# Performance work log

Hardware: AMD Instinct MI355X
Metric: run time of the kernel (lower is better)

Reference implementation:

```python
import jax, jax.numpy as jnp
import numpy as np

INPUT_SIZE = 784
HIDDEN_SIZE = 256
NUM_CLASSES = 10
BATCH = 32768


def setup_inputs() -> dict:
    key = jax.random.key(0)
    k_x, k_w1, k_b1, k_w2, k_b2 = jax.random.split(key, 5)
    return {
        "x": jax.random.normal(k_x, (BATCH, INPUT_SIZE), dtype=jnp.float32),
        "fc1_weight": jax.random.normal(k_w1, (HIDDEN_SIZE, INPUT_SIZE), dtype=jnp.float32),
        "fc1_bias": jax.random.normal(k_b1, (HIDDEN_SIZE,), dtype=jnp.float32),
        "fc2_weight": jax.random.normal(k_w2, (NUM_CLASSES, HIDDEN_SIZE), dtype=jnp.float32),
        "fc2_bias": jax.random.normal(k_b2, (NUM_CLASSES,), dtype=jnp.float32),
    }


def reference(x, fc1_weight, fc1_bias, fc2_weight, fc2_bias):
    # hidden = x @ W1^T + b1, ReLU
    hidden = jnp.einsum("bi,hi->bh", x, fc1_weight) + fc1_bias
    activated = jnp.maximum(hidden, 0.0)
    # output = activated @ W2^T + b2
    logits = jnp.einsum("bh,ch->bc", activated, fc2_weight) + fc2_bias
    return jax.nn.softmax(logits, axis=-1)
```

## Files before the change

kernel.cpp:

```cpp
#include <hip/hip_runtime.h>
#include <math.h>

#define BATCH_N   32768
#define IN_F      784
#define HID_F     256
#define NCLS      10
#define BM        64
#define NTHREADS  512

typedef __attribute__((ext_vector_type(8))) short short8;
typedef __attribute__((ext_vector_type(4))) float f32x4;

#define WS_W1H 0
#define WS_W1L 409600

union S8U { short8 s; uint4 u; };

__device__ __forceinline__ void cvt8(float4 a, float4 b, short8* hi, short8* lo) {
    const unsigned M = 0xFFFF0000u;
    const unsigned ux = __float_as_uint(a.x), uy = __float_as_uint(a.y),
                   uz = __float_as_uint(a.z), uw = __float_as_uint(a.w),
                   vx = __float_as_uint(b.x), vy = __float_as_uint(b.y),
                   vz = __float_as_uint(b.z), vw = __float_as_uint(b.w);
    S8U h, l;
    h.u.x = (ux >> 16) | (uy & M);
    h.u.y = (uz >> 16) | (uw & M);
    h.u.z = (vx >> 16) | (vy & M);
    h.u.w = (vz >> 16) | (vw & M);
    const float rx = a.x - __uint_as_float(ux & M);
    const float ry = a.y - __uint_as_float(uy & M);
    const float rz = a.z - __uint_as_float(uz & M);
    const float rw = a.w - __uint_as_float(uw & M);
    const float sx = b.x - __uint_as_float(vx & M);
    const float sy = b.y - __uint_as_float(vy & M);
    const float sz = b.z - __uint_as_float(vz & M);
    const float sw_ = b.w - __uint_as_float(vw & M);
    l.u.x = (__float_as_uint(rx) >> 16) | (__float_as_uint(ry) & M);
    l.u.y = (__float_as_uint(rz) >> 16) | (__float_as_uint(rw) & M);
    l.u.z = (__float_as_uint(sx) >> 16) | (__float_as_uint(sy) & M);
    l.u.w = (__float_as_uint(sz) >> 16) | (__float_as_uint(sw_) & M);
    *hi = h.s; *lo = l.s;
}

__global__ __launch_bounds__(256)
void prep_w1_kernel(const float* __restrict__ w1, char* __restrict__ ws) {
    const int s    = blockIdx.x * 256 + threadIdx.x;
    const int lane = s & 63, ct = (s >> 6) & 15, kt = s >> 10;
    const int n    = ct * 16 + (lane & 15);
    const int k0   = kt * 32 + (lane >> 4) * 8;
    float4 a = make_float4(0.f, 0.f, 0.f, 0.f), b = a;
    if (k0 + 7 < IN_F) {
        const float* p = w1 + (size_t)n * IN_F + k0;
        a = *(const float4*)p;
        b = *(const float4*)(p + 4);
    }
    short8 hi, lo;
    cvt8(a, b, &hi, &lo);
    *(short8*)(ws + WS_W1H + (size_t)s * 16) = hi;
    *(short8*)(ws + WS_W1L + (size_t)s * 16) = lo;
}

__device__ __forceinline__ void gload16(const void* g, void* l) {
    __builtin_amdgcn_global_load_lds(
        (const __attribute__((address_space(1))) void*)g,
        (__attribute__((address_space(3))) void*)l, 16, 0, 0);
}

__device__ __forceinline__ short8 gload_s8(const void* p) {
    short8 r;
    asm volatile("global_load_dwordx4 %0, %1, off" : "=v"(r) : "v"(p));
    return r;
}

__global__ __launch_bounds__(NTHREADS, 2)
void mlp_mfma_kernel(const float* __restrict__ x,
                     const char*  __restrict__ wsb,
                     const float* __restrict__ b1,
                     const float* __restrict__ w2,
                     const float* __restrict__ b2,
                     float* __restrict__ out)
{
    __shared__ char  xraw[4][8192];
    __shared__ float hid[64 * 128];

    const int tid  = threadIdx.x;
    const int lane = tid & 63;
    const int wv   = tid >> 6;
    const int wc   = wv & 3;
    const int wr   = wv >> 2;
    const int m    = lane & 15;
    const int quad = lane >> 4;
    const int row0 = blockIdx.x * BM;

    const int srow = wv * 8 + (lane >> 3);
    const int gch  = (lane & 7) ^ (lane >> 3);
    const float* xg = x + (size_t)(row0 + srow) * IN_F;

    const int msw = m & 7;
    const int rowbase = (wr * 32 + m) * 128;
    const int o0 = ((2 * quad)     ^ msw) * 16;
    const int o1 = ((2 * quad + 1) ^ msw) * 16;

    const char* bhp = wsb + WS_W1H + ((size_t)(wc * 4) * 64 + lane) * 16;
    const char* blp = wsb + WS_W1L + ((size_t)(wc * 4) * 64 + lane) * 16;

    f32x4 acc[2][4];
    #pragma unroll
    for (int a = 0; a < 2; ++a)
        #pragma unroll
        for (int b = 0; b < 4; ++b)
            acc[a][b] = (f32x4){0.f, 0.f, 0.f, 0.f};

    gload16(xg + gch * 4,      &xraw[0][wv * 1024]);
    gload16(xg + 32 + gch * 4, &xraw[1][wv * 1024]);
    short8 bhc[4], blc[4], bhn[4], bln[4];
    #pragma unroll
    for (int c = 0; c < 4; ++c) {
        bhc[c] = gload_s8(bhp + c * 1024);
        blc[c] = gload_s8(blp + c * 1024);
    }

    for (int kb = 0; kb < 24; kb += 4) {
        #pragma unroll
        for (int i = 0; i < 4; ++i) {
            const int kt = kb + i;
            {
                const int ktc = (kt + 2 > 24) ? 24 : kt + 2;
                const int cgc = (ktc == 24 && gch > 3) ? 0 : gch;
                gload16(xg + ktc * 32 + cgc * 4, &xraw[(i + 2) & 3][wv * 1024]);
            }
            #pragma unroll
            for (int c = 0; c < 4; ++c) {
                bhn[c] = gload_s8(bhp + (size_t)(kt + 1) * 16384 + c * 1024);
                bln[c] = gload_s8(blp + (size_t)(kt + 1) * 16384 + c * 1024);
            }
            asm volatile("s_waitcnt vmcnt(9)");
            __builtin_amdgcn_sched_barrier(0);
            __builtin_amdgcn_s_barrier();
            __builtin_amdgcn_sched_barrier(0);
            const char* xr = &xraw[i][0];
            __builtin_amdgcn_s_setprio(1);
            #pragma unroll
            for (int rt = 0; rt < 2; ++rt) {
                const float4 fa = *(const float4*)(xr + rowbase + rt * 2048 + o0);
                const float4 fb = *(const float4*)(xr + rowbase + rt * 2048 + o1);
                short8 ah, al;
                cvt8(fa, fb, &ah, &al);
                #pragma unroll
                for (int c = 0; c < 4; ++c) {
                    acc[rt][c] = __builtin_amdgcn_mfma_f32_16x16x32_bf16(ah, bhc[c], acc[rt][c], 0, 0, 0);
                    acc[rt][c] = __builtin_amdgcn_mfma_f32_16x16x32_bf16(al, bhc[c], acc[rt][c], 0, 0, 0);
                    acc[rt][c] = __builtin_amdgcn_mfma_f32_16x16x32_bf16(ah, blc[c], acc[rt][c], 0, 0, 0);
                }
            }
            __builtin_amdgcn_s_setprio(0);
            #pragma unroll
            for (int c = 0; c < 4; ++c) { bhc[c] = bhn[c]; blc[c] = bln[c]; }
        }
    }

    {
        asm volatile("s_waitcnt vmcnt(0)");
        __builtin_amdgcn_sched_barrier(0);
        __builtin_amdgcn_s_barrier();
        __builtin_amdgcn_sched_barrier(0);
        const char* xr = &xraw[0][0];
        __builtin_amdgcn_s_setprio(1);
        #pragma unroll
        for (int rt = 0; rt < 2; ++rt) {
            const float4 fa = *(const float4*)(xr + rowbase + rt * 2048 + o0);
            const float4 fb = *(const float4*)(xr + rowbase + rt * 2048 + o1);
            short8 ah, al;
            cvt8(fa, fb, &ah, &al);
            if (quad >= 2) {
                const short8 zz = {0, 0, 0, 0, 0, 0, 0, 0};
                ah = zz; al = zz;
            }
            #pragma unroll
            for (int c = 0; c < 4; ++c) {
                acc[rt][c] = __builtin_amdgcn_mfma_f32_16x16x32_bf16(ah, bhc[c], acc[rt][c], 0, 0, 0);
                acc[rt][c] = __builtin_amdgcn_mfma_f32_16x16x32_bf16(al, bhc[c], acc[rt][c], 0, 0, 0);
                acc[rt][c] = __builtin_amdgcn_mfma_f32_16x16x32_bf16(ah, blc[c], acc[rt][c], 0, 0, 0);
            }
        }
        __builtin_amdgcn_s_setprio(0);
    }

    const int rl    = tid >> 3;
    const int slice = tid & 7;
    const int gb    = (slice >> 1) * 64 + (slice & 1) * 16;
    const int cb    = slice * 16;
    const int sw2   = (rl & 7) << 2;

    float lg[NCLS];
    #pragma unroll
    for (int k = 0; k < NCLS; ++k) lg[k] = 0.f;

    #pragma unroll
    for (int p = 0; p < 2; ++p) {
        if (p) __syncthreads();
        #pragma unroll
        for (int cl = 0; cl < 2; ++cl) {
            const int c  = 2 * p + cl;
            const int g  = (wc * 4 + c) * 16 + m;
            const float bv = b1[g];
            const int cc = wc * 32 + cl * 16 + m;
            #pragma unroll
            for (int rt = 0; rt < 2; ++rt)
                #pragma unroll
                for (int reg = 0; reg < 4; ++reg) {
                    const int row = wr * 32 + rt * 16 + quad * 4 + reg;
                    hid[row * 128 + (cc ^ ((row & 7) << 2))] =
                        fmaxf(acc[rt][c][reg] + bv, 0.f);
                }
        }
        __syncthreads();
        #pragma unroll
        for (int i = 0; i < 4; ++i) {
            const float4 h = *(const float4*)(hid + rl * 128 + ((cb + i * 4) ^ sw2));
            const int g4 = gb + 32 * p + i * 4;
            #pragma unroll
            for (int k = 0; k < NCLS; ++k) {
                const float4 w = *(const float4*)(w2 + k * HID_F + g4);
                lg[k] += h.x * w.x + h.y * w.y + h.z * w.z + h.w * w.w;
            }
        }
    }

    #pragma unroll
    for (int k = 0; k < NCLS; ++k) {
        float v = lg[k];
        v += __shfl_xor(v, 1);
        v += __shfl_xor(v, 2);
        v += __shfl_xor(v, 4);
        lg[k] = v + b2[k];
    }
    float mx = -1e30f;
    #pragma unroll
    for (int k = 0; k < NCLS; ++k) mx = fmaxf(mx, lg[k]);
    float s = 0.f;
    #pragma unroll
    for (int k = 0; k < NCLS; ++k) { lg[k] = __expf(lg[k] - mx); s += lg[k]; }
    const float inv = 1.f / s;
    const float va = (slice & 4)
        ? ((slice & 2) ? ((slice & 1) ? lg[7] : lg[6]) : ((slice & 1) ? lg[5] : lg[4]))
        : ((slice & 2) ? ((slice & 1) ? lg[3] : lg[2]) : ((slice & 1) ? lg[1] : lg[0]));
    const float vb = (slice & 1) ? lg[9] : lg[8];
    float* o = out + (size_t)(row0 + rl) * NCLS;
    o[slice] = va * inv;
    if (slice < 2) o[8 + slice] = vb * inv;
}

extern "C" void kernel_launch(void* const* d_in, const int* in_sizes, int n_in,
                              void* d_out, int out_size, void* d_ws, size_t ws_size,
                              hipStream_t stream)
{
    const float* x  = (const float*)d_in[0];
    const float* w1 = (const float*)d_in[1];
    const float* b1 = (const float*)d_in[2];
    const float* w2 = (const float*)d_in[3];
    const float* b2 = (const float*)d_in[4];
    float* out = (float*)d_out;

    hipLaunchKernelGGL(prep_w1_kernel, dim3(100), dim3(256), 0, stream,
                       w1, (char*)d_ws);
    hipLaunchKernelGGL(mlp_mfma_kernel, dim3(BATCH_N / BM), dim3(NTHREADS), 0, stream,
                       x, (const char*)d_ws, b1, w2, b2, out);
}
```

Measured before the change: 215.8 us.

## Convert x tile to bf16 hi/lo once in LDS and retile waves by columns

Each wave now owns 32 hidden columns across all 64 rows instead of a 2x4 row/column split. The fp32 x tile is converted into bf16 hi/lo halves once per block into double-buffered LDS, so waves no longer convert the same rows redundantly. The pipeline adds a 3-stage register rotation for W1 fragments and a 4-deep x prefetch. Launch bounds now request 4 blocks per CU, and LDS is unioned with the hidden buffer so the full 256-wide hidden tile is stored once. The extra LDS traffic and tighter register budget may offset the savings.

```diff
diff --git a/kernel.cpp b/kernel.cpp
--- a/kernel.cpp
+++ b/kernel.cpp
@@ -42,6 +42,20 @@
     *hi = h.s; *lo = l.s;
 }
 
+__device__ __forceinline__ void cvt4(float4 a, uint2* h, uint2* l) {
+    const unsigned M = 0xFFFF0000u;
+    const unsigned ux = __float_as_uint(a.x), uy = __float_as_uint(a.y),
+                   uz = __float_as_uint(a.z), uw = __float_as_uint(a.w);
+    h->x = (ux >> 16) | (uy & M);
+    h->y = (uz >> 16) | (uw & M);
+    const float rx = a.x - __uint_as_float(ux & M);
+    const float ry = a.y - __uint_as_float(uy & M);
+    const float rz = a.z - __uint_as_float(uz & M);
+    const float rw = a.w - __uint_as_float(uw & M);
+    l->x = (__float_as_uint(rx) >> 16) | (__float_as_uint(ry) & M);
+    l->y = (__float_as_uint(rz) >> 16) | (__float_as_uint(rw) & M);
+}
+
 __global__ __launch_bounds__(256)
 void prep_w1_kernel(const float* __restrict__ w1, char* __restrict__ ws) {
     const int s    = blockIdx.x * 256 + threadIdx.x;
@@ -72,7 +86,7 @@
     return r;
 }
 
-__global__ __launch_bounds__(NTHREADS, 2)
+__global__ __launch_bounds__(NTHREADS, 4)
 void mlp_mfma_kernel(const float* __restrict__ x,
                      const char*  __restrict__ wsb,
                      const float* __restrict__ b1,
@@ -80,14 +94,18 @@
                      const float* __restrict__ b2,
                      float* __restrict__ out)
 {
-    __shared__ char  xraw[4][8192];
-    __shared__ float hid[64 * 128];
+    __shared__ union {
+        struct {
+            char raw[4][8192];
+            char convh[2][4096];
+            char convl[2][4096];
+        } s;
+        float hid[64 * 256];
+    } sm;
 
     const int tid  = threadIdx.x;
     const int lane = tid & 63;
     const int wv   = tid >> 6;
-    const int wc   = wv & 3;
-    const int wr   = wv >> 2;
     const int m    = lane & 15;
     const int quad = lane >> 4;
     const int row0 = blockIdx.x * BM;
@@ -96,137 +114,154 @@
     const int gch  = (lane & 7) ^ (lane >> 3);
     const float* xg = x + (size_t)(row0 + srow) * IN_F;
 
-    const int msw = m & 7;
-    const int rowbase = (wr * 32 + m) * 128;
-    const int o0 = ((2 * quad)     ^ msw) * 16;
-    const int o1 = ((2 * quad + 1) ^ msw) * 16;
-
-    const char* bhp = wsb + WS_W1H + ((size_t)(wc * 4) * 64 + lane) * 16;
-    const char* blp = wsb + WS_W1L + ((size_t)(wc * 4) * 64 + lane) * 16;
-
-    f32x4 acc[2][4];
-    #pragma unroll
-    for (int a = 0; a < 2; ++a)
+    const int cr  = tid >> 3;
+    const int cc  = (tid & 7) ^ (cr & 7);
+    const int cq  = cc >> 1;
+    const int conv_off = cr * 64 + ((cq ^ ((cr >> 1) & 3)) << 4) + (cc & 1) * 8;
+
+    const int fbase = m * 64 + ((quad ^ ((m >> 1) & 3)) << 4);
+
+    const char* bhp = wsb + WS_W1H + ((size_t)(wv * 2) * 64 + lane) * 16;
+    const char* blp = wsb + WS_W1L + ((size_t)(wv * 2) * 64 + lane) * 16;
+
+    f32x4 acc[4][2];
+    #pragma unroll
+    for (int a = 0; a < 4; ++a)
         #pragma unroll
-        for (int b = 0; b < 4; ++b)
+        for (int b = 0; b < 2; ++b)
             acc[a][b] = (f32x4){0.f, 0.f, 0.f, 0.f};
 
-    gload16(xg + gch * 4,      &xraw[0][wv * 1024]);
-    gload16(xg + 32 + gch * 4, &xraw[1][wv * 1024]);
-    short8 bhc[4], blc[4], bhn[4], bln[4];
-    #pragma unroll
-    for (int c = 0; c < 4; ++c) {
-        bhc[c] = gload_s8(bhp + c * 1024);
-        blc[c] = gload_s8(blp + c * 1024);
-    }
-
-    for (int kb = 0; kb < 24; kb += 4) {
-        #pragma unroll
-        for (int i = 0; i < 4; ++i) {
-            const int kt = kb + i;
-            {
-                const int ktc = (kt + 2 > 24) ? 24 : kt + 2;
-                const int cgc = (ktc == 24 && gch > 3) ? 0 : gch;
-                gload16(xg + ktc * 32 + cgc * 4, &xraw[(i + 2) & 3][wv * 1024]);
-            }
-            #pragma unroll
-            for (int c = 0; c < 4; ++c) {
-                bhn[c] = gload_s8(bhp + (size_t)(kt + 1) * 16384 + c * 1024);
-                bln[c] = gload_s8(blp + (size_t)(kt + 1) * 16384 + c * 1024);
-            }
-            asm volatile("s_waitcnt vmcnt(9)");
-            __builtin_amdgcn_sched_barrier(0);
-            __builtin_amdgcn_s_barrier();
-            __builtin_amdgcn_sched_barrier(0);
-            const char* xr = &xraw[i][0];
-            __builtin_amdgcn_s_setprio(1);
-            #pragma unroll
-            for (int rt = 0; rt < 2; ++rt) {
-                const float4 fa = *(const float4*)(xr + rowbase + rt * 2048 + o0);
-                const float4 fb = *(const float4*)(xr + rowbase + rt * 2048 + o1);
-                short8 ah, al;
-                cvt8(fa, fb, &ah, &al);
-                #pragma unroll
-                for (int c = 0; c < 4; ++c) {
-                    acc[rt][c] = __builtin_amdgcn_mfma_f32_16x16x32_bf16(ah, bhc[c], acc[rt][c], 0, 0, 0);
-                    acc[rt][c] = __builtin_amdgcn_mfma_f32_16x16x32_bf16(al, bhc[c], acc[rt][c], 0, 0, 0);
-                    acc[rt][c] = __builtin_amdgcn_mfma_f32_16x16x32_bf16(ah, blc[c], acc[rt][c], 0, 0, 0);
-                }
-            }
-            __builtin_amdgcn_s_setprio(0);
-            #pragma unroll
-            for (int c = 0; c < 4; ++c) { bhc[c] = bhn[c]; blc[c] = bln[c]; }
-        }
-    }
+    short8 b0h[2], b0l[2], b1h[2], b1l[2], b2h[2], b2l[2];
+
+    gload16(xg + gch * 4,       &sm.s.raw[0][wv * 1024]);
+    gload16(xg + 32 + gch * 4,  &sm.s.raw[1][wv * 1024]);
+    gload16(xg + 64 + gch * 4,  &sm.s.raw[2][wv * 1024]);
+    b0h[0] = gload_s8(bhp);            b0h[1] = gload_s8(bhp + 1024);
+    b0l[0] = gload_s8(blp);            b0l[1] = gload_s8(blp + 1024);
+    b1h[0] = gload_s8(bhp + 16384);    b1h[1] = gload_s8(bhp + 16384 + 1024);
+    b1l[0] = gload_s8(blp + 16384);    b1l[1] = gload_s8(blp + 16384 + 1024);
+    asm volatile("s_waitcnt vmcnt(9)");
+    __builtin_amdgcn_sched_barrier(0);
+    __builtin_amdgcn_s_barrier();
+    __builtin_amdgcn_sched_barrier(0);
+    {
+        const float4 f = *(const float4*)(sm.s.raw[0] + tid * 16);
+        uint2 h, l;
+        cvt4(f, &h, &l);
+        *(uint2*)(sm.s.convh[0] + conv_off) = h;
+        *(uint2*)(sm.s.convl[0] + conv_off) = l;
+    }
+    asm volatile("s_waitcnt lgkmcnt(0)");
+    __builtin_amdgcn_sched_barrier(0);
+    __builtin_amdgcn_s_barrier();
+    __builtin_amdgcn_sched_barrier(0);
+
+#define BODY(KT, BHC, BLC, BHN, BLN)                                           \
+    {                                                                          \
+        const int kt = (KT);                                                   \
+        const int kx = (kt + 3 > 24) ? 24 : kt + 3;                            \
+        const int cg = (kx == 24 && gch > 3) ? 0 : gch;                        \
+        gload16(xg + kx * 32 + cg * 4, &sm.s.raw[(kt + 3) & 3][wv * 1024]);    \
+        const int kb2 = (kt + 2 > 24) ? 24 : kt + 2;                           \
+        const char* bhq = bhp + (size_t)kb2 * 16384;                           \
+        const char* blq = blp + (size_t)kb2 * 16384;                           \
+        BHN[0] = gload_s8(bhq);  BHN[1] = gload_s8(bhq + 1024);                \
+        BLN[0] = gload_s8(blq);  BLN[1] = gload_s8(blq + 1024);                \
+        asm volatile("s_waitcnt vmcnt(9)");                                    \
+        __builtin_amdgcn_sched_barrier(0);                                     \
+        {                                                                      \
+            const float4 f = *(const float4*)(sm.s.raw[(kt + 1) & 3] + tid * 16); \
+            uint2 h, l;                                                        \
+            cvt4(f, &h, &l);                                                   \
+            *(uint2*)(sm.s.convh[(kt + 1) & 1] + conv_off) = h;                \
+            *(uint2*)(sm.s.convl[(kt + 1) & 1] + conv_off) = l;                \
+        }                                                                      \
+        {                                                                      \
+            const char* ch  = sm.s.convh[kt & 1];                              \
+            const char* cl2 = sm.s.convl[kt & 1];                              \
+            __builtin_amdgcn_s_setprio(1);                                     \
+            _Pragma("unroll")                                                  \
+            for (int rt = 0; rt < 4; ++rt) {                                   \
+                const short8 ah = *(const short8*)(ch  + fbase + rt * 1024);   \
+                const short8 al = *(const short8*)(cl2 + fbase + rt * 1024);   \
+                _Pragma("unroll")                                              \
+                for (int c = 0; c < 2; ++c) {                                  \
+                    acc[rt][c] = __builtin_amdgcn_mfma_f32_16x16x32_bf16(ah, BHC[c], acc[rt][c], 0, 0, 0); \
+                    acc[rt][c] = __builtin_amdgcn_mfma_f32_16x16x32_bf16(al, BHC[c], acc[rt][c], 0, 0, 0); \
+                    acc[rt][c] = __builtin_amdgcn_mfma_f32_16x16x32_bf16(ah, BLC[c], acc[rt][c], 0, 0, 0); \
+                }                                                              \
+            }                                                                  \
+            __builtin_amdgcn_s_setprio(0);                                     \
+        }                                                                      \
+        asm volatile("s_waitcnt lgkmcnt(0)");                                  \
+        __builtin_amdgcn_sched_barrier(0);                                     \
+        __builtin_amdgcn_s_barrier();                                          \
+        __builtin_amdgcn_sched_barrier(0);                                     \
+    }
+
+    for (int kb = 0; kb < 24; kb += 3) {
+        BODY(kb,     b0h, b0l, b2h, b2l);
+        BODY(kb + 1, b1h, b1l, b0h, b0l);
+        BODY(kb + 2, b2h, b2l, b1h, b1l);
+    }
+#undef BODY
 
     {
         asm volatile("s_waitcnt vmcnt(0)");
         __builtin_amdgcn_sched_barrier(0);
-        __builtin_amdgcn_s_barrier();
-        __builtin_amdgcn_sched_barrier(0);
-        const char* xr = &xraw[0][0];
+        const char* ch  = sm.s.convh[0];
+        const char* cl2 = sm.s.convl[0];
         __builtin_amdgcn_s_setprio(1);
         #pragma unroll
-        for (int rt = 0; rt < 2; ++rt) {
-            const float4 fa = *(const float4*)(xr + rowbase + rt * 2048 + o0);
-            const float4 fb = *(const float4*)(xr + rowbase + rt * 2048 + o1);
-            short8 ah, al;
-            cvt8(fa, fb, &ah, &al);
+        for (int rt = 0; rt < 4; ++rt) {
+            short8 ah = *(const short8*)(ch  + fbase + rt * 1024);
+            short8 al = *(const short8*)(cl2 + fbase + rt * 1024);
             if (quad >= 2) {
                 const short8 zz = {0, 0, 0, 0, 0, 0, 0, 0};
                 ah = zz; al = zz;
             }
             #pragma unroll
-            for (int c = 0; c < 4; ++c) {
-                acc[rt][c] = __builtin_amdgcn_mfma_f32_16x16x32_bf16(ah, bhc[c], acc[rt][c], 0, 0, 0);
-                acc[rt][c] = __builtin_amdgcn_mfma_f32_16x16x32_bf16(al, bhc[c], acc[rt][c], 0, 0, 0);
-                acc[rt][c] = __builtin_amdgcn_mfma_f32_16x16x32_bf16(ah, blc[c], acc[rt][c], 0, 0, 0);
+            for (int c = 0; c < 2; ++c) {
+                acc[rt][c] = __builtin_amdgcn_mfma_f32_16x16x32_bf16(ah, b0h[c], acc[rt][c], 0, 0, 0);
+                acc[rt][c] = __builtin_amdgcn_mfma_f32_16x16x32_bf16(al, b0h[c], acc[rt][c], 0, 0, 0);
+                acc[rt][c] = __builtin_amdgcn_mfma_f32_16x16x32_bf16(ah, b0l[c], acc[rt][c], 0, 0, 0);
             }
         }
         __builtin_amdgcn_s_setprio(0);
     }
 
+    __syncthreads();
+    #pragma unroll
+    for (int c = 0; c < 2; ++c) {
+        const int g  = (wv * 2 + c) * 16 + m;
+        const float bv = b1[g];
+        #pragma unroll
+        for (int rt = 0; rt < 4; ++rt)
+            #pragma unroll
+            for (int reg = 0; reg < 4; ++reg) {
+                const int row = rt * 16 + quad * 4 + reg;
+                sm.hid[row * 256 + (g ^ ((row & 7) << 2))] =
+                    fmaxf(acc[rt][c][reg] + bv, 0.f);
+            }
+    }
+    __syncthreads();
+
     const int rl    = tid >> 3;
     const int slice = tid & 7;
-    const int gb    = (slice >> 1) * 64 + (slice & 1) * 16;
-    const int cb    = slice * 16;
     const int sw2   = (rl & 7) << 2;
-
     float lg[NCLS];
     #pragma unroll
     for (int k = 0; k < NCLS; ++k) lg[k] = 0.f;
-
-    #pragma unroll
-    for (int p = 0; p < 2; ++p) {
-        if (p) __syncthreads();
+    #pragma unroll
+    for (int i = 0; i < 8; ++i) {
+        const int col = slice * 32 + i * 4;
+        const float4 h = *(const float4*)(sm.hid + rl * 256 + (col ^ sw2));
         #pragma unroll
-        for (int cl = 0; cl < 2; ++cl) {
-            const int c  = 2 * p + cl;
-            const int g  = (wc * 4 + c) * 16 + m;
-            const float bv = b1[g];
-            const int cc = wc * 32 + cl * 16 + m;
-            #pragma unroll
-            for (int rt = 0; rt < 2; ++rt)
-                #pragma unroll
-                for (int reg = 0; reg < 4; ++reg) {
-                    const int row = wr * 32 + rt * 16 + quad * 4 + reg;
-                    hid[row * 128 + (cc ^ ((row & 7) << 2))] =
-                        fmaxf(acc[rt][c][reg] + bv, 0.f);
-                }
+        for (int k = 0; k < NCLS; ++k) {
+            const float4 w = *(const float4*)(w2 + k * HID_F + col);
+            lg[k] += h.x * w.x + h.y * w.y + h.z * w.z + h.w * w.w;
         }
-        __syncthreads();
-        #pragma unroll
-        for (int i = 0; i < 4; ++i) {
-            const float4 h = *(const float4*)(hid + rl * 128 + ((cb + i * 4) ^ sw2));
-            const int g4 = gb + 32 * p + i * 4;
-            #pragma unroll
-            for (int k = 0; k < NCLS; ++k) {
-                const float4 w = *(const float4*)(w2 + k * HID_F + g4);
-                lg[k] += h.x * w.x + h.y * w.y + h.z * w.z + h.w * w.w;
-            }
-        }
-    }
-
+    }
     #pragma unroll
     for (int k = 0; k < NCLS; ++k) {
         float v = lg[k];
```

Result: no change. 213.5 us (-1.0%).

## Switch to 32x32x16 MFMA with register-staged, pre-split bf16 x tiles

Applied to the files above, without the earlier changes.

Replaces the 16x16x32 MFMA tiling with 32x32x16 bf16 MFMAs, where each wave owns 32 hidden columns across all 64 rows. x is now loaded into registers, converted once into bf16 hi/lo, and stored in a double-buffered LDS stage, so each element is converted once instead of once per wave. Barriers drop to one per 7 k-steps instead of one per k-step. The W1 prep layout is reworked to match, and the second layer now runs in a single pass over a 256-wide hidden buffer. In exchange, the x prefetch is shorter, wave 7 sits idle during staging, and waitcnt accounting is tighter.

```diff
diff --git a/kernel.cpp b/kernel.cpp
--- a/kernel.cpp
+++ b/kernel.cpp
@@ -8,11 +8,12 @@
 #define BM        64
 #define NTHREADS  512
 
-typedef __attribute__((ext_vector_type(8))) short short8;
-typedef __attribute__((ext_vector_type(4))) float f32x4;
+typedef __attribute__((ext_vector_type(8)))  short short8;
+typedef __attribute__((ext_vector_type(4)))  float f32x4;
+typedef __attribute__((ext_vector_type(16))) float f32x16;
 
 #define WS_W1H 0
-#define WS_W1L 409600
+#define WS_W1L 401408
 
 union S8U { short8 s; uint4 u; };
 
@@ -42,35 +43,39 @@
     *hi = h.s; *lo = l.s;
 }
 
+__device__ __forceinline__ void cvt8v(f32x4 a, f32x4 b, short8* hi, short8* lo) {
+    float4 fa = make_float4(a[0], a[1], a[2], a[3]);
+    float4 fb = make_float4(b[0], b[1], b[2], b[3]);
+    cvt8(fa, fb, hi, lo);
+}
+
 __global__ __launch_bounds__(256)
 void prep_w1_kernel(const float* __restrict__ w1, char* __restrict__ ws) {
     const int s    = blockIdx.x * 256 + threadIdx.x;
-    const int lane = s & 63, ct = (s >> 6) & 15, kt = s >> 10;
-    const int n    = ct * 16 + (lane & 15);
-    const int k0   = kt * 32 + (lane >> 4) * 8;
-    float4 a = make_float4(0.f, 0.f, 0.f, 0.f), b = a;
-    if (k0 + 7 < IN_F) {
-        const float* p = w1 + (size_t)n * IN_F + k0;
-        a = *(const float4*)p;
-        b = *(const float4*)(p + 4);
-    }
+    const int lane = s & 63, ct = (s >> 6) & 7, kt = s >> 9;
+    const int n    = ct * 32 + (lane & 31);
+    const int k0   = kt * 16 + (lane >> 5) * 8;
+    const float* p = w1 + (size_t)n * IN_F + k0;
+    const float4 a = *(const float4*)p;
+    const float4 b = *(const float4*)(p + 4);
     short8 hi, lo;
     cvt8(a, b, &hi, &lo);
     *(short8*)(ws + WS_W1H + (size_t)s * 16) = hi;
     *(short8*)(ws + WS_W1L + (size_t)s * 16) = lo;
 }
 
-__device__ __forceinline__ void gload16(const void* g, void* l) {
-    __builtin_amdgcn_global_load_lds(
-        (const __attribute__((address_space(1))) void*)g,
-        (__attribute__((address_space(3))) void*)l, 16, 0, 0);
-}
-
 __device__ __forceinline__ short8 gload_s8(const void* p) {
     short8 r;
     asm volatile("global_load_dwordx4 %0, %1, off" : "=v"(r) : "v"(p));
     return r;
 }
+__device__ __forceinline__ f32x4 gload_f4(const float* p) {
+    f32x4 r;
+    asm volatile("global_load_dwordx4 %0, %1, off" : "=v"(r) : "v"(p));
+    return r;
+}
+
+#define MFMA32(A, B, C) __builtin_amdgcn_mfma_f32_32x32x16_bf16((A), (B), (C), 0, 0, 0)
 
 __global__ __launch_bounds__(NTHREADS, 2)
 void mlp_mfma_kernel(const float* __restrict__ x,
@@ -80,153 +85,155 @@
                      const float* __restrict__ b2,
                      float* __restrict__ out)
 {
-    __shared__ char  xraw[4][8192];
-    __shared__ float hid[64 * 128];
-
-    const int tid  = threadIdx.x;
-    const int lane = tid & 63;
-    const int wv   = tid >> 6;
-    const int wc   = wv & 3;
-    const int wr   = wv >> 2;
-    const int m    = lane & 15;
-    const int quad = lane >> 4;
-    const int row0 = blockIdx.x * BM;
-
-    const int srow = wv * 8 + (lane >> 3);
-    const int gch  = (lane & 7) ^ (lane >> 3);
-    const float* xg = x + (size_t)(row0 + srow) * IN_F;
-
-    const int msw = m & 7;
-    const int rowbase = (wr * 32 + m) * 128;
-    const int o0 = ((2 * quad)     ^ msw) * 16;
-    const int o1 = ((2 * quad + 1) ^ msw) * 16;
-
-    const char* bhp = wsb + WS_W1H + ((size_t)(wc * 4) * 64 + lane) * 16;
-    const char* blp = wsb + WS_W1L + ((size_t)(wc * 4) * 64 + lane) * 16;
-
-    f32x4 acc[2][4];
-    #pragma unroll
-    for (int a = 0; a < 2; ++a)
+    __shared__ union {
+        char  stage[2][28672];
+        float hid[64 * 256];
+    } sm;
+
+    const int tid   = threadIdx.x;
+    const int lane  = tid & 63;
+    const int wv    = tid >> 6;
+    const int l31   = lane & 31;
+    const int khalf = lane >> 5;
+    const int row0  = blockIdx.x * BM;
+
+    const int srow  = tid & 63;
+    const int sktl  = (wv < 7) ? wv : 6;
+    const float* xs = x + (size_t)(row0 + srow) * IN_F + sktl * 16;
+    const int ssw   = (srow >> 2) & 1;
+    const int swo0  = sktl * 2048 + srow * 32 + (0 ^ ssw) * 16;
+    const int swo1  = sktl * 2048 + srow * 32 + (1 ^ ssw) * 16;
+
+    const int asw = (l31 >> 2) & 1;
+    const int aro = l31 * 32 + ((khalf ^ asw) << 4);
+
+    const char* bhp = wsb + WS_W1H + ((size_t)wv * 64 + lane) * 16;
+    const char* blp = wsb + WS_W1L + ((size_t)wv * 64 + lane) * 16;
+
+    f32x16 acc0, acc1;
+    #pragma unroll
+    for (int r = 0; r < 16; ++r) { acc0[r] = 0.f; acc1[r] = 0.f; }
+
+    f32x4 s0 = gload_f4(xs), s1 = gload_f4(xs + 4),
+          s2 = gload_f4(xs + 8), s3 = gload_f4(xs + 12);
+    short8 bh0, bl0, bh1, bl1;
+    bh0 = gload_s8(bhp);
+    bl0 = gload_s8(blp);
+    asm volatile("s_waitcnt vmcnt(2)" ::: "memory");
+    __builtin_amdgcn_sched_barrier(0);
+    if (wv < 7) {
+        short8 h0, l0, h1, l1;
+        cvt8v(s0, s1, &h0, &l0);
+        cvt8v(s2, s3, &h1, &l1);
+        char* st = sm.stage[0];
+        *(short8*)(st + swo0)         = h0;
+        *(short8*)(st + 14336 + swo0) = l0;
+        *(short8*)(st + swo1)         = h1;
+        *(short8*)(st + 14336 + swo1) = l1;
+    }
+    asm volatile("s_waitcnt lgkmcnt(0)" ::: "memory");
+    __builtin_amdgcn_sched_barrier(0);
+    __builtin_amdgcn_s_barrier();
+    __builtin_amdgcn_sched_barrier(0);
+
+    #pragma unroll
+    for (int g = 0; g < 7; ++g) {
+        const char* bufr = sm.stage[g & 1];
         #pragma unroll
-        for (int b = 0; b < 4; ++b)
-            acc[a][b] = (f32x4){0.f, 0.f, 0.f, 0.f};
-
-    gload16(xg + gch * 4,      &xraw[0][wv * 1024]);
-    gload16(xg + 32 + gch * 4, &xraw[1][wv * 1024]);
-    short8 bhc[4], blc[4], bhn[4], bln[4];
-    #pragma unroll
-    for (int c = 0; c < 4; ++c) {
-        bhc[c] = gload_s8(bhp + c * 1024);
-        blc[c] = gload_s8(blp + c * 1024);
-    }
-
-    for (int kb = 0; kb < 24; kb += 4) {
+        for (int t = 0; t < 7; ++t) {
+            const int kt = g * 7 + t;
+            if (kt < 48) {
+                const char* pbh = bhp + (size_t)(kt + 1) * 8192;
+                const char* pbl = blp + (size_t)(kt + 1) * 8192;
+                if (kt & 1) { bh0 = gload_s8(pbh); bl0 = gload_s8(pbl); }
+                else        { bh1 = gload_s8(pbh); bl1 = gload_s8(pbl); }
+            }
+            if (g < 6 && t == 4) {
+                const float* sp = xs + (g + 1) * 112;
+                s0 = gload_f4(sp);      s1 = gload_f4(sp + 4);
+                s2 = gload_f4(sp + 8);  s3 = gload_f4(sp + 12);
+            }
+            if (g < 6 && (t == 4 || t == 5)) {
+                asm volatile("s_waitcnt vmcnt(6)" ::: "memory");
+            } else if (kt == 48) {
+                asm volatile("s_waitcnt vmcnt(0)" ::: "memory");
+            } else {
+                asm volatile("s_waitcnt vmcnt(2)" ::: "memory");
+            }
+            __builtin_amdgcn_sched_barrier(0);
+            const short8 ah0 = *(const short8*)(bufr + t * 2048 + aro);
+            const short8 al0 = *(const short8*)(bufr + 14336 + t * 2048 + aro);
+            const short8 ah1 = *(const short8*)(bufr + t * 2048 + aro + 1024);
+            const short8 al1 = *(const short8*)(bufr + 14336 + t * 2048 + aro + 1024);
+            __builtin_amdgcn_s_setprio(1);
+            if (kt & 1) {
+                acc0 = MFMA32(ah0, bh1, acc0);
+                acc0 = MFMA32(al0, bh1, acc0);
+                acc0 = MFMA32(ah0, bl1, acc0);
+                acc1 = MFMA32(ah1, bh1, acc1);
+                acc1 = MFMA32(al1, bh1, acc1);
+                acc1 = MFMA32(ah1, bl1, acc1);
+            } else {
+                acc0 = MFMA32(ah0, bh0, acc0);
+                acc0 = MFMA32(al0, bh0, acc0);
+                acc0 = MFMA32(ah0, bl0, acc0);
+                acc1 = MFMA32(ah1, bh0, acc1);
+                acc1 = MFMA32(al1, bh0, acc1);
+                acc1 = MFMA32(ah1, bl0, acc1);
+            }
+            __builtin_amdgcn_s_setprio(0);
+            __builtin_amdgcn_sched_barrier(0);
+        }
+        if (g < 6) {
+            if (wv < 7) {
+                short8 h0, l0, h1, l1;
+                cvt8v(s0, s1, &h0, &l0);
+                cvt8v(s2, s3, &h1, &l1);
+                char* st = sm.stage[(g + 1) & 1];
+                *(short8*)(st + swo0)         = h0;
+                *(short8*)(st + 14336 + swo0) = l0;
+                *(short8*)(st + swo1)         = h1;
+                *(short8*)(st + 14336 + swo1) = l1;
+            }
+            asm volatile("s_waitcnt lgkmcnt(0)" ::: "memory");
+            __builtin_amdgcn_sched_barrier(0);
+            __builtin_amdgcn_s_barrier();
+            __builtin_amdgcn_sched_barrier(0);
+        }
+    }
+
+    __syncthreads();
+    {
+        const int col = wv * 32 + l31;
+        const float bv = b1[col];
         #pragma unroll
-        for (int i = 0; i < 4; ++i) {
-            const int kt = kb + i;
-            {
-                const int ktc = (kt + 2 > 24) ? 24 : kt + 2;
-                const int cgc = (ktc == 24 && gch > 3) ? 0 : gch;
-                gload16(xg + ktc * 32 + cgc * 4, &xraw[(i + 2) & 3][wv * 1024]);
-            }
-            #pragma unroll
-            for (int c = 0; c < 4; ++c) {
-                bhn[c] = gload_s8(bhp + (size_t)(kt + 1) * 16384 + c * 1024);
-                bln[c] = gload_s8(blp + (size_t)(kt + 1) * 16384 + c * 1024);
-            }
-            asm volatile("s_waitcnt vmcnt(9)");
-            __builtin_amdgcn_sched_barrier(0);
-            __builtin_amdgcn_s_barrier();
-            __builtin_amdgcn_sched_barrier(0);
-            const char* xr = &xraw[i][0];
-            __builtin_amdgcn_s_setprio(1);
-            #pragma unroll
-            for (int rt = 0; rt < 2; ++rt) {
-                const float4 fa = *(const float4*)(xr + rowbase + rt * 2048 + o0);
-                const float4 fb = *(const float4*)(xr + rowbase + rt * 2048 + o1);
-                short8 ah, al;
-                cvt8(fa, fb, &ah, &al);
-                #pragma unroll
-                for (int c = 0; c < 4; ++c) {
-                    acc[rt][c] = __builtin_amdgcn_mfma_f32_16x16x32_bf16(ah, bhc[c], acc[rt][c], 0, 0, 0);
-                    acc[rt][c] = __builtin_amdgcn_mfma_f32_16x16x32_bf16(al, bhc[c], acc[rt][c], 0, 0, 0);
-                    acc[rt][c] = __builtin_amdgcn_mfma_f32_16x16x32_bf16(ah, blc[c], acc[rt][c], 0, 0, 0);
-                }
-            }
-            __builtin_amdgcn_s_setprio(0);
-            #pragma unroll
-            for (int c = 0; c < 4; ++c) { bhc[c] = bhn[c]; blc[c] = bln[c]; }
-        }
-    }
-
-    {
-        asm volatile("s_waitcnt vmcnt(0)");
-        __builtin_amdgcn_sched_barrier(0);
-        __builtin_amdgcn_s_barrier();
-        __builtin_amdgcn_sched_barrier(0);
-        const char* xr = &xraw[0][0];
-        __builtin_amdgcn_s_setprio(1);
-        #pragma unroll
-        for (int rt = 0; rt < 2; ++rt) {
-            const float4 fa = *(const float4*)(xr + rowbase + rt * 2048 + o0);
-            const float4 fb = *(const float4*)(xr + rowbase + rt * 2048 + o1);
-            short8 ah, al;
-            cvt8(fa, fb, &ah, &al);
-            if (quad >= 2) {
-                const short8 zz = {0, 0, 0, 0, 0, 0, 0, 0};
-                ah = zz; al = zz;
-            }
-            #pragma unroll
-            for (int c = 0; c < 4; ++c) {
-                acc[rt][c] = __builtin_amdgcn_mfma_f32_16x16x32_bf16(ah, bhc[c], acc[rt][c], 0, 0, 0);
-                acc[rt][c] = __builtin_amdgcn_mfma_f32_16x16x32_bf16(al, bhc[c], acc[rt][c], 0, 0, 0);
-                acc[rt][c] = __builtin_amdgcn_mfma_f32_16x16x32_bf16(ah, blc[c], acc[rt][c], 0, 0, 0);
-            }
-        }
-        __builtin_amdgcn_s_setprio(0);
-    }
+        for (int reg = 0; reg < 16; ++reg) {
+            const int rowb = (reg & 3) + 8 * (reg >> 2) + 4 * khalf;
+            sm.hid[rowb * 256 + (col ^ ((rowb & 7) << 2))] =
+                fmaxf(acc0[reg] + bv, 0.f);
+            const int rowc = 32 + rowb;
+            sm.hid[rowc * 256 + (col ^ ((rowc & 7) << 2))] =
+                fmaxf(acc1[reg] + bv, 0.f);
+        }
+    }
+    __syncthreads();
 
     const int rl    = tid >> 3;
     const int slice = tid & 7;
-    const int gb    = (slice >> 1) * 64 + (slice & 1) * 16;
-    const int cb    = slice * 16;
     const int sw2   = (rl & 7) << 2;
-
     float lg[NCLS];
     #pragma unroll
     for (int k = 0; k < NCLS; ++k) lg[k] = 0.f;
-
-    #pragma unroll
-    for (int p = 0; p < 2; ++p) {
-        if (p) __syncthreads();
+    #pragma unroll
+    for (int i = 0; i < 8; ++i) {
+        const int col = slice * 32 + i * 4;
+        const float4 h = *(const float4*)(sm.hid + rl * 256 + (col ^ sw2));
         #pragma unroll
-        for (int cl = 0; cl < 2; ++cl) {
-            const int c  = 2 * p + cl;
-            const int g  = (wc * 4 + c) * 16 + m;
-            const float bv = b1[g];
-            const int cc = wc * 32 + cl * 16 + m;
-            #pragma unroll
-            for (int rt = 0; rt < 2; ++rt)
-                #pragma unroll
-                for (int reg = 0; reg < 4; ++reg) {
-                    const int row = wr * 32 + rt * 16 + quad * 4 + reg;
-                    hid[row * 128 + (cc ^ ((row & 7) << 2))] =
-                        fmaxf(acc[rt][c][reg] + bv, 0.f);
-                }
-        }
-        __syncthreads();
-        #pragma unroll
-        for (int i = 0; i < 4; ++i) {
-            const float4 h = *(const float4*)(hid + rl * 128 + ((cb + i * 4) ^ sw2));
-            const int g4 = gb + 32 * p + i * 4;
-            #pragma unroll
-            for (int k = 0; k < NCLS; ++k) {
-                const float4 w = *(const float4*)(w2 + k * HID_F + g4);
-                lg[k] += h.x * w.x + h.y * w.y + h.z * w.z + h.w * w.w;
-            }
-        }
-    }
-
+        for (int k = 0; k < NCLS; ++k) {
+            const float4 w = *(const float4*)(w2 + k * HID_F + col);
+            lg[k] += h.x * w.x + h.y * w.y + h.z * w.z + h.w * w.w;
+        }
+    }
     #pragma unroll
     for (int k = 0; k < NCLS; ++k) {
         float v = lg[k];
@@ -262,7 +269,7 @@
     const float* b2 = (const float*)d_in[4];
     float* out = (float*)d_out;
 
-    hipLaunchKernelGGL(prep_w1_kernel, dim3(100), dim3(256), 0, stream,
+    hipLaunchKernelGGL(prep_w1_kernel, dim3(98), dim3(256), 0, stream,
                        w1, (char*)d_ws);
     hipLaunchKernelGGL(mlp_mfma_kernel, dim3(BATCH_N / BM), dim3(NTHREADS), 0, stream,
                        x, (const char*)d_ws, b1, w2, b2, out);
```

New measurement: 213.2 us. Within noise of the previous version (-1.2%).
